# Kernel tuning notes

Measured on AMD Instinct MI355X. Metric: run time of the kernel, lower is better.

Reference implementation:

```python
import jax, jax.numpy as jnp
import numpy as np

D = 384      # pct_dim == spm_dim == d_model
H = 6        # heads
DK = D // H  # 64
HID = 96     # int(384 * 0.25)
B = 8
NS = 2040    # multiple of 85 (SPM pyramid 64+16+4+1 groups)
NP = 2048


def _ln(x, g, b, eps):
    m = x.mean(-1, keepdims=True)
    v = jnp.mean((x - m) ** 2, -1, keepdims=True)
    return (x - m) * jax.lax.rsqrt(v + eps) * g + b


def setup_inputs() -> dict:
    key = jax.random.key(0)
    ks = jax.random.split(key, 10)
    w = lambda k, shape: jax.random.normal(k, shape, jnp.float32) * 0.02
    p = {
        "spm_feature": jax.random.normal(ks[0], (B, NS, D), jnp.float32),
        "pct_feature": jax.random.normal(ks[1], (B, NP, D), jnp.float32),
        # extractor pre-norms (eps=1e-6)
        "pct_g": jnp.ones(D), "pct_b": jnp.zeros(D),
        "spm_g": jnp.ones(D), "spm_b": jnp.zeros(D),
        # CrossAttention internal norms (eps=1e-5)
        "lnx_g": jnp.ones(D), "lnx_b": jnp.zeros(D),
        "lny_g": jnp.ones(D), "lny_b": jnp.zeros(D),
        "Wq": w(ks[2], (D, D)), "bq": jnp.zeros(D),
        "Wk": w(ks[3], (D, D)), "bk": jnp.zeros(D),
        "Wv": w(ks[4], (D, D)), "bv": jnp.zeros(D),
        # 1x1 Conv1d in CrossAttention
        "Wc": w(ks[5], (D, D)), "bc": jnp.zeros(D),
        "lnc_g": jnp.ones(D), "lnc_b": jnp.zeros(D),
        # FFN
        "ffn_g": jnp.ones(D), "ffn_b": jnp.zeros(D),
        "W1": w(ks[6], (HID, D)), "b1": jnp.zeros(HID),
        "Wdw": w(ks[7], (HID, HID)), "bdw": jnp.zeros(HID),
        "W2": w(ks[8], (D, HID)), "b2": jnp.zeros(D),
    }
    return p


def reference(spm_feature, pct_feature, pct_g, pct_b, spm_g, spm_b,
              lnx_g, lnx_b, lny_g, lny_b, Wq, bq, Wk, bk, Wv, bv,
              Wc, bc, lnc_g, lnc_b, ffn_g, ffn_b, W1, b1, Wdw, bdw, W2, b2):
    EPS6, EPS5 = 1e-6, 1e-5
    # extractor pre-norms (the (N,B,C) permutes in the torch code cancel for LN)
    x = _ln(spm_feature, spm_g, spm_b, EPS6)
    y = _ln(pct_feature, pct_g, pct_b, EPS6)
    # CrossAttention's own (double) LayerNorms
    xn = _ln(x, lnx_g, lnx_b, EPS5)
    yn = _ln(y, lny_g, lny_b, EPS5)
    Bq, Nq, _ = xn.shape
    q = (xn @ Wq.T + bq).reshape(Bq, Nq, H, DK)
    k = (yn @ Wk.T + bk).reshape(Bq, -1, H, DK)
    v = (yn @ Wv.T + bv).reshape(Bq, -1, H, DK)
    scale = 1.0 / np.sqrt(DK).astype(np.float32)
    scores = jnp.einsum('bqhd,bkhd->bhqk', q, k) * scale
    att = jax.nn.softmax(scores, axis=-1)
    # non-standard extra renormalization across the HEAD dimension (dim=1)
    att = att / (1e-9 + att.sum(axis=1, keepdims=True))
    o = jnp.einsum('bhqk,bkhd->bqhd', att, v).reshape(Bq, Nq, D)
    qf = q.reshape(Bq, Nq, D)
    r = (qf - o) @ Wc.T + bc            # 1x1 Conv1d == channel linear
    r = _ln(r, lnc_g, lnc_b, EPS5)
    r = jnp.where(r > 0, r, 0.02 * r)    # LeakyReLU(0.02)
    cross = qf + r
    spm = spm_feature + cross            # first residual
    # FFN: fc1 -> (4-way segment split, shared 1x1 dwconv1, concat) -> gelu -> fc2
    # a 1x1 Conv1d with shared weights applied to contiguous segments then
    # concatenated is mathematically identical to one application on the full seq
    h = _ln(spm, ffn_g, ffn_b, EPS5)
    h = h @ W1.T + b1                    # (B, NS, 96)
    h = h @ Wdw.T + bdw                  # shared 1x1 conv over channels
    h = jax.nn.gelu(h, approximate=False)
    h = h @ W2.T + b2                    # (B, NS, 384)
    return spm + h
```

## Files before the change

### kernel.cpp

```cpp
#include <hip/hip_runtime.h>
#include <hip/hip_bf16.h>
#include <math.h>

#define D 384
#define NHEAD 6
#define DKH 64
#define HID 96
#define BB 8
#define NS 2040
#define NPK 2048

typedef __attribute__((ext_vector_type(8))) short short8;
typedef __attribute__((ext_vector_type(4))) short short4v;
typedef __attribute__((ext_vector_type(4))) float f32x4;

__device__ __forceinline__ float bf2f(ushort u) {
  union { uint u; float f; } x; x.u = ((uint)u) << 16; return x.f;
}
__device__ __forceinline__ ushort f2bf(float f) {
  union { float f; uint u; } x; x.f = f;
  uint r = x.u + 0x7fffu + ((x.u >> 16) & 1u);
  return (ushort)(r >> 16);
}
__device__ __forceinline__ float ldin(const void* p, size_t i, bool f32) {
  return f32 ? ((const float*)p)[i] : bf2f(((const ushort*)p)[i]);
}
__device__ __forceinline__ float2 ld2in(const void* p, size_t i, bool f32) {
  if (f32) return *(const float2*)((const float*)p + i);
  uint w = *(const uint*)((const ushort*)p + i);
  return make_float2(bf2f((ushort)(w & 0xffffu)), bf2f((ushort)(w >> 16)));
}
__device__ __forceinline__ uint4 load8bf(const void* p, size_t off, bool f32) {
  if (!f32) return *(const uint4*)((const ushort*)p + off);
  const float* f = (const float*)p + off;
  float4 a = *(const float4*)f, b = *(const float4*)(f + 4);
  uint4 r;
  r.x = (uint)f2bf(a.x) | ((uint)f2bf(a.y) << 16);
  r.y = (uint)f2bf(a.z) | ((uint)f2bf(a.w) << 16);
  r.z = (uint)f2bf(b.x) | ((uint)f2bf(b.y) << 16);
  r.w = (uint)f2bf(b.z) | ((uint)f2bf(b.w) << 16);
  return r;
}
__device__ __forceinline__ uint bfsub3(uint a, uint p0, uint p1) {
  float lo = bf2f((ushort)(a & 0xffffu)) - (bf2f((ushort)(p0 & 0xffffu)) + bf2f((ushort)(p1 & 0xffffu)));
  float hi = bf2f((ushort)(a >> 16))     - (bf2f((ushort)(p0 >> 16))     + bf2f((ushort)(p1 >> 16)));
  return (uint)f2bf(lo) | ((uint)f2bf(hi) << 16);
}

__global__ void probe_dtype(const void* ones_vec, int* flg) {
  if (threadIdx.x == 0 && blockIdx.x == 0) {
    uint u = *(const uint*)ones_vec;
    *flg = (u == 0x3F800000u) ? 1 : 0;
  }
}

__global__ __launch_bounds__(256) void ln2_kernel(
    const void* __restrict__ src,
    const void* __restrict__ g1, const void* __restrict__ b1,
    const void* __restrict__ g2, const void* __restrict__ b2,
    ushort* __restrict__ dst, const int* __restrict__ flg,
    int rows, float eps1, float eps2)
{
  const bool f32 = *flg != 0;
  int row = blockIdx.x * 4 + (threadIdx.x >> 6);
  int lane = threadIdx.x & 63;
  if (row >= rows) return;
  float v[6];
#pragma unroll
  for (int j = 0; j < 3; ++j) {
    int c = 2 * (lane + 64 * j);
    float2 w = ld2in(src, (size_t)row * D + c, f32);
    v[2*j] = w.x; v[2*j+1] = w.y;
  }
  float s = 0.f, s2 = 0.f;
#pragma unroll
  for (int i = 0; i < 6; ++i) { s += v[i]; s2 += v[i]*v[i]; }
#pragma unroll
  for (int off = 32; off; off >>= 1) { s += __shfl_xor(s, off); s2 += __shfl_xor(s2, off); }
  float mean = s * (1.f/D);
  float rstd = rsqrtf(fmaxf(s2*(1.f/D) - mean*mean, 0.f) + eps1);
  float t[6];
  float u = 0.f, u2 = 0.f;
#pragma unroll
  for (int j = 0; j < 3; ++j) {
    int c = 2 * (lane + 64 * j);
    float2 g = ld2in(g1, c, f32), bb = ld2in(b1, c, f32);
    float v0 = (v[2*j]   - mean) * rstd * g.x + bb.x;
    float v1 = (v[2*j+1] - mean) * rstd * g.y + bb.y;
    t[2*j] = v0; t[2*j+1] = v1;
    u += v0 + v1; u2 += v0*v0 + v1*v1;
  }
#pragma unroll
  for (int off = 32; off; off >>= 1) { u += __shfl_xor(u, off); u2 += __shfl_xor(u2, off); }
  float mean2 = u * (1.f/D);
  float rstd2 = rsqrtf(fmaxf(u2*(1.f/D) - mean2*mean2, 0.f) + eps2);
  ushort* q = dst + (size_t)row * D;
#pragma unroll
  for (int j = 0; j < 3; ++j) {
    int c = 2 * (lane + 64 * j);
    float2 g = ld2in(g2, c, f32), bb = ld2in(b2, c, f32);
    ushort lo = f2bf((t[2*j]   - mean2) * rstd2 * g.x + bb.x);
    ushort hi = f2bf((t[2*j+1] - mean2) * rstd2 * g.y + bb.y);
    *(uint*)(q + c) = (uint)lo | ((uint)hi << 16);
  }
}

template<int EPI>
__global__ __launch_bounds__(256) void gemm_bt(
    const ushort* __restrict__ A,
    const void* __restrict__ W, const void* __restrict__ bias,
    void* __restrict__ Cout,
    const int* __restrict__ flg, int M, int N, int K)
{
  const bool f32 = *flg != 0;
  __shared__ ushort As[64][40];
  __shared__ ushort Ws[64][40];
  int tm = blockIdx.x * 64, tn = blockIdx.y * 64;
  int tid = threadIdx.x;
  int wv = tid >> 6, lane = tid & 63;
  f32x4 acc[4] = {{0,0,0,0},{0,0,0,0},{0,0,0,0},{0,0,0,0}};
  int lrow = tid >> 2, lc8 = (tid & 3) * 8;
  for (int k0 = 0; k0 < K; k0 += 32) {
    __syncthreads();
    uint4 aval = *(const uint4*)(A + (size_t)(tm + lrow) * K + k0 + lc8);
    *(uint4*)&As[lrow][lc8] = aval;
    uint4 wval = make_uint4(0,0,0,0);
    int wr = tn + lrow;
    if (wr < N) wval = load8bf(W, (size_t)wr * K + k0 + lc8, f32);
    *(uint4*)&Ws[lrow][lc8] = wval;
    __syncthreads();
    short8 af = *(const short8*)&As[16*wv + (lane & 15)][8*(lane >> 4)];
#pragma unroll
    for (int n = 0; n < 4; ++n) {
      short8 bfr = *(const short8*)&Ws[16*n + (lane & 15)][8*(lane >> 4)];
      acc[n] = __builtin_amdgcn_mfma_f32_16x16x32_bf16(af, bfr, acc[n], 0, 0, 0);
    }
  }
  int rbase = tm + 16*wv + 4*(lane >> 4);
#pragma unroll
  for (int n = 0; n < 4; ++n) {
    int col = tn + 16*n + (lane & 15);
    if (col >= N) continue;
    float bv = ldin(bias, col, f32);
#pragma unroll
    for (int e = 0; e < 4; ++e) {
      int row = rbase + e;
      float val = acc[n][e] + bv;
      if (EPI == 1) val = 0.5f * val * (1.f + erff(val * 0.70710678118654752f));
      ((ushort*)Cout)[(size_t)row * N + col] = f2bf(val);
    }
  }
}

template<int EPI, int ASUB>
__global__ __launch_bounds__(256) void gemm12864(
    const ushort* __restrict__ A, const ushort* __restrict__ A2,
    const ushort* __restrict__ A3,
    const void* __restrict__ W, const void* __restrict__ bias,
    const ushort* __restrict__ resid, void* __restrict__ Cout,
    const int* __restrict__ flg, int M, int N, int K)
{
  const bool f32 = *flg != 0;
  __shared__ ushort As[128][40];
  __shared__ ushort Bs[64][40];
  int tm = blockIdx.x * 128, tn = blockIdx.y * 64;
  int tid = threadIdx.x;
  int wv = tid >> 6, lane = tid & 63;
  int l15 = lane & 15, l4 = lane >> 4;
  f32x4 acc[2][4];
#pragma unroll
  for (int m = 0; m < 2; ++m)
#pragma unroll
    for (int n = 0; n < 4; ++n) acc[m][n] = f32x4{0.f,0.f,0.f,0.f};
  int br = tid >> 2, bc8 = (tid & 3) * 8;
  for (int k0 = 0; k0 < K; k0 += 32) {
    __syncthreads();
#pragma unroll
    for (int i = 0; i < 2; ++i) {
      int idx = tid + 256*i;
      int r = idx >> 2, c8 = (idx & 3) * 8;
      int ar = tm + r; if (ar > M-1) ar = M-1;
      uint4 aval = *(const uint4*)(A + (size_t)ar * K + k0 + c8);
      if (ASUB) {
        uint4 bval = *(const uint4*)(A2 + (size_t)ar * K + k0 + c8);
        uint4 cval = *(const uint4*)(A3 + (size_t)ar * K + k0 + c8);
        aval.x = bfsub3(aval.x, bval.x, cval.x); aval.y = bfsub3(aval.y, bval.y, cval.y);
        aval.z = bfsub3(aval.z, bval.z, cval.z); aval.w = bfsub3(aval.w, bval.w, cval.w);
      }
      *(uint4*)&As[r][c8] = aval;
    }
    uint4 wvl = load8bf(W, (size_t)(tn + br) * K + k0 + bc8, f32);
    *(uint4*)&Bs[br][bc8] = wvl;
    __syncthreads();
    short8 af[2], bfv[4];
#pragma unroll
    for (int m = 0; m < 2; ++m) af[m] = *(const short8*)&As[wv*32 + m*16 + l15][l4*8];
#pragma unroll
    for (int n = 0; n < 4; ++n) bfv[n] = *(const short8*)&Bs[n*16 + l15][l4*8];
#pragma unroll
    for (int m = 0; m < 2; ++m)
#pragma unroll
      for (int n = 0; n < 4; ++n)
        acc[m][n] = __builtin_amdgcn_mfma_f32_16x16x32_bf16(af[m], bfv[n], acc[m][n], 0, 0, 0);
  }
#pragma unroll
  for (int n = 0; n < 4; ++n) {
    int col = tn + n*16 + l15;
    float bv = ldin(bias, col, f32);
#pragma unroll
    for (int m = 0; m < 2; ++m) {
#pragma unroll
      for (int e = 0; e < 4; ++e) {
        int row = tm + wv*32 + m*16 + 4*l4 + e;
        if (row >= M) continue;
        float val = acc[m][n][e] + bv;
        if (EPI == 2) val += bf2f(resid[(size_t)row * N + col]);
        if (EPI == 2 && f32) {
          ((float*)Cout)[(size_t)row * N + col] = val;
        } else {
          ((ushort*)Cout)[(size_t)row * N + col] = f2bf(val);
        }
      }
    }
  }
}

__global__ __launch_bounds__(256) void vt_tr(
    const ushort* __restrict__ v, ushort* __restrict__ vt)
{
  __shared__ ushort T[64][66];
  int k0 = blockIdx.x * 64, d0 = blockIdx.y * 64, b = blockIdx.z;
  int tid = threadIdx.x;
#pragma unroll
  for (int i = 0; i < 2; ++i) {
    int f = tid + 256*i;
    int r = f >> 3, c8 = (f & 7) * 8;
    uint4 w = *(const uint4*)(v + (size_t)(b*NPK + k0 + r)*D + d0 + c8);
    const ushort* wsp = (const ushort*)&w;
#pragma unroll
    for (int j = 0; j < 8; ++j) T[r][c8 + j] = wsp[j];
  }
  __syncthreads();
#pragma unroll
  for (int i = 0; i < 2; ++i) {
    int f = tid + 256*i;
    int r = f >> 3, c8 = (f & 7) * 8;
    ushort tmp[8];
#pragma unroll
    for (int j = 0; j < 8; ++j) tmp[j] = T[c8 + j][r];
    *(uint4*)(vt + (size_t)(b*D + d0 + r)*NPK + k0 + c8) = *(const uint4*)tmp;
  }
}

__global__ __launch_bounds__(256) void attn_mz(
    const ushort* __restrict__ q, const ushort* __restrict__ k,
    float* __restrict__ mmout)
{
  __shared__ ushort Ksh[64][72];
  int qt = blockIdx.x, h = blockIdx.y, b = blockIdx.z;
  int tid = threadIdx.x, wv = tid >> 6, lane = tid & 63;
  int l15 = lane & 15, l4 = lane >> 4;
  int q0 = qt*64 + wv*16;
  const float C = 0.18033688011112042f;
  int qrow = q0 + l15; if (qrow > NS-1) qrow = NS-1;
  const ushort* qp = q + (size_t)(b*NS + qrow)*D + h*64 + l4*8;
  short8 qf0 = *(const short8*)(qp);
  short8 qf1 = *(const short8*)(qp + 32);
  float m[4] = {-1e30f,-1e30f,-1e30f,-1e30f};
  float z[4] = {0.f,0.f,0.f,0.f};
  for (int kt = 0; kt < NPK; kt += 64) {
    __syncthreads();
#pragma unroll
    for (int i = 0; i < 2; ++i) {
      int f = tid + 256*i;
      int r = f >> 3, c8 = (f & 7) * 8;
      *(uint4*)&Ksh[r][c8] = *(const uint4*)(k + (size_t)(b*NPK + kt + r)*D + h*64 + c8);
    }
    __syncthreads();
#pragma unroll
    for (int ks = 0; ks < 4; ++ks) {
      short8 b0 = *(const short8*)&Ksh[ks*16 + l15][l4*8];
      short8 b1 = *(const short8*)&Ksh[ks*16 + l15][32 + l4*8];
      f32x4 t = {0.f,0.f,0.f,0.f};
      t = __builtin_amdgcn_mfma_f32_16x16x32_bf16(qf0, b0, t, 0, 0, 0);
      t = __builtin_amdgcn_mfma_f32_16x16x32_bf16(qf1, b1, t, 0, 0, 0);
#pragma unroll
      for (int e = 0; e < 4; ++e) {
        float u = t[e] * C;
        float mn = fmaxf(m[e], u);
        z[e] = z[e]*exp2f(m[e]-mn) + exp2f(u-mn);
        m[e] = mn;
      }
    }
  }
#pragma unroll
  for (int off = 1; off < 16; off <<= 1) {
#pragma unroll
    for (int e = 0; e < 4; ++e) {
      float mo = __shfl_xor(m[e], off);
      float zo = __shfl_xor(z[e], off);
      float mn = fmaxf(m[e], mo);
      z[e] = z[e]*exp2f(m[e]-mn) + zo*exp2f(mo-mn);
      m[e] = mn;
    }
  }
  if (l15 == 0) {
#pragma unroll
    for (int e = 0; e < 4; ++e) {
      int row = q0 + l4*4 + e;
      if (row < NS) mmout[(size_t)(b*NHEAD + h)*NS + row] = m[e] + log2f(z[e]);
    }
  }
}

__global__ __launch_bounds__(256, 2) void attn_pv(
    const ushort* __restrict__ q, const ushort* __restrict__ k,
    const ushort* __restrict__ vt, const float* __restrict__ mm,
    ushort* __restrict__ op0, ushort* __restrict__ op1)
{
  __shared__ ushort Ks[32][392];
  __shared__ ushort Vt[384][36];
  int wgid = blockIdx.x;
  int b = wgid & 7, qt = (wgid >> 3) & 31, sl = wgid >> 8;
  ushort* opart = sl ? op1 : op0;
  int tid = threadIdx.x, wv = tid >> 6, lane = tid & 63;
  int l15 = lane & 15, l4 = lane >> 4;
  int q0 = qt*64 + wv*16;
  const float C = 0.18033688011112042f;
  int qrow = q0 + l15; if (qrow > NS-1) qrow = NS-1;
  short8 qf[12];
#pragma unroll
  for (int c = 0; c < 12; ++c)
    qf[c] = *(const short8*)(q + (size_t)(b*NS + qrow)*D + c*32 + l4*8);
  float mmr[6];
#pragma unroll
  for (int h = 0; h < 6; ++h)
    mmr[h] = mm[(size_t)(b*NHEAD + h)*NS + qrow];
  f32x4 acc[6][4];
#pragma unroll
  for (int h = 0; h < 6; ++h)
#pragma unroll
    for (int n = 0; n < 4; ++n) acc[h][n] = f32x4{0.f,0.f,0.f,0.f};

  for (int kt = sl*1024; kt < sl*1024 + 1024; kt += 32) {
    __syncthreads();
#pragma unroll
    for (int i = 0; i < 6; ++i) {
      int f = tid + 256*i;
      int r = f / 48, c = (f % 48) * 8;
      *(uint4*)&Ks[r][c] = *(const uint4*)(k + (size_t)(b*NPK + kt + r)*D + c);
    }
#pragma unroll
    for (int i = 0; i < 6; ++i) {
      int f = tid + 256*i;
      int r = f >> 2, c8 = (f & 3) * 8;
      uint4 wv4 = *(const uint4*)(vt + (size_t)(b*D + r)*NPK + kt + c8);
      *(uint2*)&Vt[r][c8]     = make_uint2(wv4.x, wv4.y);
      *(uint2*)&Vt[r][c8 + 4] = make_uint2(wv4.z, wv4.w);
    }
    __syncthreads();
    f32x4 s[6][2];
    __builtin_amdgcn_s_setprio(1);
#pragma unroll
    for (int h = 0; h < 6; ++h)
#pragma unroll
      for (int ks = 0; ks < 2; ++ks) {
        short8 a0 = *(const short8*)&Ks[ks*16 + l15][h*64 + l4*8];
        short8 a1 = *(const short8*)&Ks[ks*16 + l15][h*64 + 32 + l4*8];
        f32x4 t = {0.f,0.f,0.f,0.f};
        t = __builtin_amdgcn_mfma_f32_16x16x32_bf16(a0, qf[2*h],   t, 0, 0, 0);
        t = __builtin_amdgcn_mfma_f32_16x16x32_bf16(a1, qf[2*h+1], t, 0, 0, 0);
        s[h][ks] = t;
      }
    __builtin_amdgcn_s_setprio(0);
    short4v pa[6][2];
#pragma unroll
    for (int ks = 0; ks < 2; ++ks) {
#pragma unroll
      for (int e = 0; e < 4; ++e) {
        float w6[6];
        float sum = 1e-9f;
#pragma unroll
        for (int h = 0; h < 6; ++h) {
          w6[h] = exp2f(s[h][ks][e]*C - mmr[h]);
          sum += w6[h];
        }
        float inv = __builtin_amdgcn_rcpf(sum);
#pragma unroll
        for (int h = 0; h < 6; ++h) s[h][ks][e] = w6[h]*inv;
      }
#pragma unroll
      for (int h = 0; h < 6; ++h) {
        union { float f; uint u; } x0, x1, x2, x3;
        x0.f = s[h][ks][0]; x1.f = s[h][ks][1];
        x2.f = s[h][ks][2]; x3.f = s[h][ks][3];
        uint lo = (x1.u & 0xFFFF0000u) | (x0.u >> 16);
        uint hi = (x3.u & 0xFFFF0000u) | (x2.u >> 16);
        union { uint2 u; short4v s4; } cv;
        cv.u = make_uint2(lo, hi);
        pa[h][ks] = cv.s4;
      }
    }
    __builtin_amdgcn_s_setprio(1);
#pragma unroll
    for (int h = 0; h < 6; ++h)
#pragma unroll
      for (int n = 0; n < 4; ++n)
#pragma unroll
        for (int ks = 0; ks < 2; ++ks) {
          short4v vb4 = *(const short4v*)&Vt[h*64 + 16*n + l15][ks*16 + l4*4];
          acc[h][n] = __builtin_amdgcn_mfma_f32_16x16x16bf16_1k(pa[h][ks], vb4, acc[h][n], 0, 0, 0);
        }
    __builtin_amdgcn_s_setprio(0);
  }
#pragma unroll
  for (int h = 0; h < 6; ++h)
#pragma unroll
    for (int n = 0; n < 4; ++n)
#pragma unroll
      for (int e = 0; e < 4; ++e) {
        int row = q0 + l4*4 + e;
        if (row < NS) opart[(size_t)(b*NS + row)*D + h*64 + 16*n + l15] = f2bf(acc[h][n][e]);
      }
}

__global__ __launch_bounds__(256) void cross_ln(
    const ushort* __restrict__ rtmp, const ushort* __restrict__ q,
    const void* __restrict__ spm,
    const void* __restrict__ lg, const void* __restrict__ lb,
    const void* __restrict__ fg, const void* __restrict__ fb,
    ushort* __restrict__ spm2, ushort* __restrict__ hin,
    const int* __restrict__ flg, int rows)
{
  const bool f32 = *flg != 0;
  int row = blockIdx.x * 4 + (threadIdx.x >> 6);
  int lane = threadIdx.x & 63;
  if (row >= rows) return;
  const ushort* rp = rtmp + (size_t)row * D;
  float v[6];
#pragma unroll
  for (int j = 0; j < 3; ++j) {
    uint w = *(const uint*)(rp + 2*(lane + 64*j));
    v[2*j]   = bf2f((ushort)(w & 0xffffu));
    v[2*j+1] = bf2f((ushort)(w >> 16));
  }
  float s = 0.f, s2 = 0.f;
#pragma unroll
  for (int i = 0; i < 6; ++i) { s += v[i]; s2 += v[i]*v[i]; }
#pragma unroll
  for (int off = 32; off; off >>= 1) { s += __shfl_xor(s, off); s2 += __shfl_xor(s2, off); }
  float mean = s * (1.f/D);
  float rstd = rsqrtf(fmaxf(s2*(1.f/D) - mean*mean, 0.f) + 1e-5f);
  const ushort* qp = q + (size_t)row * D;
  ushort* op = spm2 + (size_t)row * D;
  float t[6];
  float u = 0.f, u2 = 0.f;
#pragma unroll
  for (int j = 0; j < 3; ++j) {
    int c = 2*(lane + 64*j);
    float2 g = ld2in(lg, c, f32), bb = ld2in(lb, c, f32);
    float2 sp = ld2in(spm, (size_t)row*D + c, f32);
    uint wq = *(const uint*)(qp + c);
    float r0 = (v[2*j]   - mean)*rstd*g.x + bb.x;
    float r1 = (v[2*j+1] - mean)*rstd*g.y + bb.y;
    r0 = r0 > 0.f ? r0 : 0.02f*r0;
    r1 = r1 > 0.f ? r1 : 0.02f*r1;
    float o0 = sp.x + bf2f((ushort)(wq & 0xffffu)) + r0;
    float o1 = sp.y + bf2f((ushort)(wq >> 16))     + r1;
    op[c]   = f2bf(o0);
    op[c+1] = f2bf(o1);
    t[2*j] = o0; t[2*j+1] = o1;
    u += o0 + o1; u2 += o0*o0 + o1*o1;
  }
#pragma unroll
  for (int off = 32; off; off >>= 1) { u += __shfl_xor(u, off); u2 += __shfl_xor(u2, off); }
  float mean2 = u * (1.f/D);
  float rstd2 = rsqrtf(fmaxf(u2*(1.f/D) - mean2*mean2, 0.f) + 1e-5f);
  ushort* hp = hin + (size_t)row * D;
#pragma unroll
  for (int j = 0; j < 3; ++j) {
    int c = 2*(lane + 64*j);
    float2 g = ld2in(fg, c, f32), bb = ld2in(fb, c, f32);
    ushort lo = f2bf((t[2*j]   - mean2)*rstd2*g.x + bb.x);
    ushort hi = f2bf((t[2*j+1] - mean2)*rstd2*g.y + bb.y);
    *(uint*)(hp + c) = (uint)lo | ((uint)hi << 16);
  }
}

extern "C" void kernel_launch(void* const* d_in, const int* in_sizes, int n_in,
                              void* d_out, int out_size, void* d_ws, size_t ws_size,
                              hipStream_t stream)
{
  const void* spm   = d_in[0];
  const void* pct   = d_in[1];
  const void* pct_g = d_in[2];
  const void* pct_b = d_in[3];
  const void* spm_g = d_in[4];
  const void* spm_b = d_in[5];
  const void* lnx_g = d_in[6];
  const void* lnx_b = d_in[7];
  const void* lny_g = d_in[8];
  const void* lny_b = d_in[9];
  const void* Wq = d_in[10]; const void* bq = d_in[11];
  const void* Wk = d_in[12]; const void* bk = d_in[13];
  const void* Wv = d_in[14]; const void* bv = d_in[15];
  const void* Wc = d_in[16]; const void* bc = d_in[17];
  const void* lnc_g = d_in[18]; const void* lnc_b = d_in[19];
  const void* ffn_g = d_in[20]; const void* ffn_b = d_in[21];
  const void* W1 = d_in[22];  const void* b1 = d_in[23];
  const void* Wdw = d_in[24]; const void* bdw = d_in[25];
  const void* W2 = d_in[26];  const void* b2 = d_in[27];

  char* ws = (char*)d_ws;
  int*    flg  = (int*)(ws + 0);
  ushort* kb   = (ushort*)(ws + 256);
  ushort* vb   = (ushort*)(ws + 12583168);
  ushort* qb   = (ushort*)(ws + 25166080);
  ushort* vtg  = (ushort*)(ws + 37699840);
  char*   R    = ws + 50282752;
  ushort* xn   = (ushort*)R;
  ushort* yn   = (ushort*)R;
  ushort* op1  = (ushort*)R;
  float*  mmb  = (float*)(R + 12533760);
  ushort* op0  = vb;
  ushort* rtmp = vtg;
  ushort* spm2 = kb;
  ushort* hin  = qb;
  ushort* h1   = (ushort*)R;
  ushort* h2   = (ushort*)(R + 3133440);

  const int M_S = BB * NS;
  const int M_P = BB * NPK;

  probe_dtype<<<1, 64, 0, stream>>>(pct_g, flg);
  ln2_kernel<<<M_S/4, 256, 0, stream>>>(spm, spm_g, spm_b, lnx_g, lnx_b, xn, flg, M_S, 1e-6f, 1e-5f);
  gemm12864<0,0><<<dim3(128, 6), 256, 0, stream>>>(xn, nullptr, nullptr, Wq, bq, nullptr, qb, flg, M_S, D, D);
  ln2_kernel<<<M_P/4, 256, 0, stream>>>(pct, pct_g, pct_b, lny_g, lny_b, yn, flg, M_P, 1e-6f, 1e-5f);
  gemm12864<0,0><<<dim3(128, 6), 256, 0, stream>>>(yn, nullptr, nullptr, Wk, bk, nullptr, kb, flg, M_P, D, D);
  gemm12864<0,0><<<dim3(128, 6), 256, 0, stream>>>(yn, nullptr, nullptr, Wv, bv, nullptr, vb, flg, M_P, D, D);
  vt_tr<<<dim3(NPK/64, D/64, BB), 256, 0, stream>>>(vb, vtg);
  attn_mz<<<dim3(32, NHEAD, BB), 256, 0, stream>>>(qb, kb, mmb);
  attn_pv<<<512, 256, 0, stream>>>(qb, kb, vtg, mmb, op0, op1);
  gemm12864<0,1><<<dim3(128, 6), 256, 0, stream>>>(qb, op0, op1, Wc, bc, nullptr, rtmp, flg, M_S, D, D);
  cross_ln<<<M_S/4, 256, 0, stream>>>(rtmp, qb, spm, lnc_g, lnc_b, ffn_g, ffn_b, spm2, hin, flg, M_S);
  gemm_bt<0><<<dim3(M_S/64, 2), 256, 0, stream>>>(hin, W1, b1, h1, flg, M_S, HID, D);
  gemm_bt<1><<<dim3(M_S/64, 2), 256, 0, stream>>>(h1, Wdw, bdw, h2, flg, M_S, HID, HID);
  gemm12864<2,0><<<dim3(128, 6), 256, 0, stream>>>(h2, nullptr, nullptr, W2, b2, spm2, d_out, flg, M_S, D, HID);
}
```

Measured before the change: 512.0 us.

## Split attention PV over three key slices and register-prefetch K tiles

The attention PV kernel now splits the key range into three slices instead of two, launching 768 workgroups with launch bounds raised to 3 waves per SIMD. The extra partial output goes to the output buffer as scratch, and the Wc GEMM now subtracts three partials. K tiles are prefetched into registers one iteration ahead to overlap global loads with MFMA work. In exchange the Wc GEMM reads one more partial tensor, the tighter launch bound may force register spills given the large accumulator and Q fragment arrays, and the prefetch adds register pressure.

Measured after the change: 706.0 us. 1.38x slower.

```diff
diff --git a/kernel.cpp b/kernel.cpp
--- a/kernel.cpp
+++ b/kernel.cpp
@@ -41,9 +41,11 @@
   r.w = (uint)f2bf(b.z) | ((uint)f2bf(b.w) << 16);
   return r;
 }
-__device__ __forceinline__ uint bfsub3(uint a, uint p0, uint p1) {
-  float lo = bf2f((ushort)(a & 0xffffu)) - (bf2f((ushort)(p0 & 0xffffu)) + bf2f((ushort)(p1 & 0xffffu)));
-  float hi = bf2f((ushort)(a >> 16))     - (bf2f((ushort)(p0 >> 16))     + bf2f((ushort)(p1 >> 16)));
+__device__ __forceinline__ uint bfsub4(uint a, uint p0, uint p1, uint p2) {
+  float lo = bf2f((ushort)(a & 0xffffu))
+           - (bf2f((ushort)(p0 & 0xffffu)) + bf2f((ushort)(p1 & 0xffffu)) + bf2f((ushort)(p2 & 0xffffu)));
+  float hi = bf2f((ushort)(a >> 16))
+           - (bf2f((ushort)(p0 >> 16)) + bf2f((ushort)(p1 >> 16)) + bf2f((ushort)(p2 >> 16)));
   return (uint)f2bf(lo) | ((uint)f2bf(hi) << 16);
 }
 
@@ -155,7 +157,7 @@
 template<int EPI, int ASUB>
 __global__ __launch_bounds__(256) void gemm12864(
     const ushort* __restrict__ A, const ushort* __restrict__ A2,
-    const ushort* __restrict__ A3,
+    const ushort* __restrict__ A3, const ushort* __restrict__ A4,
     const void* __restrict__ W, const void* __restrict__ bias,
     const ushort* __restrict__ resid, void* __restrict__ Cout,
     const int* __restrict__ flg, int M, int N, int K)
@@ -184,8 +186,11 @@
       if (ASUB) {
         uint4 bval = *(const uint4*)(A2 + (size_t)ar * K + k0 + c8);
         uint4 cval = *(const uint4*)(A3 + (size_t)ar * K + k0 + c8);
-        aval.x = bfsub3(aval.x, bval.x, cval.x); aval.y = bfsub3(aval.y, bval.y, cval.y);
-        aval.z = bfsub3(aval.z, bval.z, cval.z); aval.w = bfsub3(aval.w, bval.w, cval.w);
+        uint4 dval = *(const uint4*)(A4 + (size_t)ar * K + k0 + c8);
+        aval.x = bfsub4(aval.x, bval.x, cval.x, dval.x);
+        aval.y = bfsub4(aval.y, bval.y, cval.y, dval.y);
+        aval.z = bfsub4(aval.z, bval.z, cval.z, dval.z);
+        aval.w = bfsub4(aval.w, bval.w, cval.w, dval.w);
       }
       *(uint4*)&As[r][c8] = aval;
     }
@@ -313,16 +318,16 @@
   }
 }
 
-__global__ __launch_bounds__(256, 2) void attn_pv(
+__global__ __launch_bounds__(256, 3) void attn_pv(
     const ushort* __restrict__ q, const ushort* __restrict__ k,
     const ushort* __restrict__ vt, const float* __restrict__ mm,
-    ushort* __restrict__ op0, ushort* __restrict__ op1)
+    ushort* __restrict__ op0, ushort* __restrict__ op1, ushort* __restrict__ op2)
 {
   __shared__ ushort Ks[32][392];
   __shared__ ushort Vt[384][36];
   int wgid = blockIdx.x;
   int b = wgid & 7, qt = (wgid >> 3) & 31, sl = wgid >> 8;
-  ushort* opart = sl ? op1 : op0;
+  ushort* opart = sl == 0 ? op0 : (sl == 1 ? op1 : op2);
   int tid = threadIdx.x, wv = tid >> 6, lane = tid & 63;
   int l15 = lane & 15, l4 = lane >> 4;
   int q0 = qt*64 + wv*16;
@@ -342,13 +347,25 @@
 #pragma unroll
     for (int n = 0; n < 4; ++n) acc[h][n] = f32x4{0.f,0.f,0.f,0.f};
 
-  for (int kt = sl*1024; kt < sl*1024 + 1024; kt += 32) {
-    __syncthreads();
+  int t0 = (sl*64)/3, t1 = ((sl+1)*64)/3;
+  uint4 kreg[6];
+  {
+    int kt = t0*32;
 #pragma unroll
     for (int i = 0; i < 6; ++i) {
       int f = tid + 256*i;
       int r = f / 48, c = (f % 48) * 8;
-      *(uint4*)&Ks[r][c] = *(const uint4*)(k + (size_t)(b*NPK + kt + r)*D + c);
+      kreg[i] = *(const uint4*)(k + (size_t)(b*NPK + kt + r)*D + c);
+    }
+  }
+  for (int t = t0; t < t1; ++t) {
+    int kt = t*32;
+    __syncthreads();
+#pragma unroll
+    for (int i = 0; i < 6; ++i) {
+      int f = tid + 256*i;
+      int r = f / 48, c = (f % 48) * 8;
+      *(uint4*)&Ks[r][c] = kreg[i];
     }
 #pragma unroll
     for (int i = 0; i < 6; ++i) {
@@ -359,6 +376,15 @@
       *(uint2*)&Vt[r][c8 + 4] = make_uint2(wv4.z, wv4.w);
     }
     __syncthreads();
+    if (t + 1 < t1) {
+      int ktn = (t+1)*32;
+#pragma unroll
+      for (int i = 0; i < 6; ++i) {
+        int f = tid + 256*i;
+        int r = f / 48, c = (f % 48) * 8;
+        kreg[i] = *(const uint4*)(k + (size_t)(b*NPK + ktn + r)*D + c);
+      }
+    }
     f32x4 s[6][2];
     __builtin_amdgcn_s_setprio(1);
 #pragma unroll
@@ -367,10 +393,10 @@
       for (int ks = 0; ks < 2; ++ks) {
         short8 a0 = *(const short8*)&Ks[ks*16 + l15][h*64 + l4*8];
         short8 a1 = *(const short8*)&Ks[ks*16 + l15][h*64 + 32 + l4*8];
-        f32x4 t = {0.f,0.f,0.f,0.f};
-        t = __builtin_amdgcn_mfma_f32_16x16x32_bf16(a0, qf[2*h],   t, 0, 0, 0);
-        t = __builtin_amdgcn_mfma_f32_16x16x32_bf16(a1, qf[2*h+1], t, 0, 0, 0);
-        s[h][ks] = t;
+        f32x4 t2 = {0.f,0.f,0.f,0.f};
+        t2 = __builtin_amdgcn_mfma_f32_16x16x32_bf16(a0, qf[2*h],   t2, 0, 0, 0);
+        t2 = __builtin_amdgcn_mfma_f32_16x16x32_bf16(a1, qf[2*h+1], t2, 0, 0, 0);
+        s[h][ks] = t2;
       }
     __builtin_amdgcn_s_setprio(0);
     short4v pa[6][2];
@@ -523,6 +549,7 @@
   ushort* op1  = (ushort*)R;
   float*  mmb  = (float*)(R + 12533760);
   ushort* op0  = vb;
+  ushort* op2  = (ushort*)d_out;
   ushort* rtmp = vtg;
   ushort* spm2 = kb;
   ushort* hin  = qb;
@@ -534,16 +561,16 @@
 
   probe_dtype<<<1, 64, 0, stream>>>(pct_g, flg);
   ln2_kernel<<<M_S/4, 256, 0, stream>>>(spm, spm_g, spm_b, lnx_g, lnx_b, xn, flg, M_S, 1e-6f, 1e-5f);
-  gemm12864<0,0><<<dim3(128, 6), 256, 0, stream>>>(xn, nullptr, nullptr, Wq, bq, nullptr, qb, flg, M_S, D, D);
+  gemm12864<0,0><<<dim3(128, 6), 256, 0, stream>>>(xn, nullptr, nullptr, nullptr, Wq, bq, nullptr, qb, flg, M_S, D, D);
   ln2_kernel<<<M_P/4, 256, 0, stream>>>(pct, pct_g, pct_b, lny_g, lny_b, yn, flg, M_P, 1e-6f, 1e-5f);
-  gemm12864<0,0><<<dim3(128, 6), 256, 0, stream>>>(yn, nullptr, nullptr, Wk, bk, nullptr, kb, flg, M_P, D, D);
-  gemm12864<0,0><<<dim3(128, 6), 256, 0, stream>>>(yn, nullptr, nullptr, Wv, bv, nullptr, vb, flg, M_P, D, D);
+  gemm12864<0,0><<<dim3(128, 6), 256, 0, stream>>>(yn, nullptr, nullptr, nullptr, Wk, bk, nullptr, kb, flg, M_P, D, D);
+  gemm12864<0,0><<<dim3(128, 6), 256, 0, stream>>>(yn, nullptr, nullptr, nullptr, Wv, bv, nullptr, vb, flg, M_P, D, D);
   vt_tr<<<dim3(NPK/64, D/64, BB), 256, 0, stream>>>(vb, vtg);
   attn_mz<<<dim3(32, NHEAD, BB), 256, 0, stream>>>(qb, kb, mmb);
-  attn_pv<<<512, 256, 0, stream>>>(qb, kb, vtg, mmb, op0, op1);
-  gemm12864<0,1><<<dim3(128, 6), 256, 0, stream>>>(qb, op0, op1, Wc, bc, nullptr, rtmp, flg, M_S, D, D);
+  attn_pv<<<768, 256, 0, stream>>>(qb, kb, vtg, mmb, op0, op1, op2);
+  gemm12864<0,1><<<dim3(128, 6), 256, 0, stream>>>(qb, op0, op1, op2, Wc, bc, nullptr, rtmp, flg, M_S, D, D);
   cross_ln<<<M_S/4, 256, 0, stream>>>(rtmp, qb, spm, lnc_g, lnc_b, ffn_g, ffn_b, spm2, hin, flg, M_S);
   gemm_bt<0><<<dim3(M_S/64, 2), 256, 0, stream>>>(hin, W1, b1, h1, flg, M_S, HID, D);
   gemm_bt<1><<<dim3(M_S/64, 2), 256, 0, stream>>>(h1, Wdw, bdw, h2, flg, M_S, HID, HID);
-  gemm12864<2,0><<<dim3(128, 6), 256, 0, stream>>>(h2, nullptr, nullptr, W2, b2, spm2, d_out, flg, M_S, D, HID);
-}
+  gemm12864<2,0><<<dim3(128, 6), 256, 0, stream>>>(h2, nullptr, nullptr, nullptr, W2, b2, spm2, d_out, flg, M_S, D, HID);
+}
```
